# Performance work log

Measured on AMD Instinct MI355X. Metric: run time of the kernel, lower is better.

Reference implementation:

```python
import jax, jax.numpy as jnp
import numpy as np


def _ap_class_loss(s_plus, s_minus):
    """AP rank loss for one class.

    s_plus:  [P] positive scores sorted DESCENDING (grads flow through sort gather)
    s_minus: [N] negative scores sorted ASCENDING  (grads flow through sort gather)

    The original torch code computes the optimal interleaving rank of each
    negative with a recursive quickselect divide-and-conquer. Because the
    optimal rank is monotone in the negative's score (the property the
    divide-and-conquer exploits), each negative's rank can equivalently be
    computed independently: for the negative of ascending rank j (1-indexed),
    delta_k = 1/(P*(j+k)) - 2*(s_plus[k-1] - s_minus[j-1])/(P*N),  k=1..P,
    opt_j = argmax over r in [1, P+1] of sum_{k>=r} delta_k (first max on ties),
    which is exactly opt_j() evaluated on the full range.
    """
    P = s_plus.shape[0]
    N = s_minus.shape[0]
    Pf, Nf = float(P), float(N)
    j = jnp.arange(1, N + 1, dtype=jnp.float32)[:, None]   # [N,1] ascending rank
    k = jnp.arange(1, P + 1, dtype=jnp.float32)[None, :]   # [1,P]
    # delta[m, k-1] for negative m (ascending) vs positive k (descending)
    delta = (1.0 / (j + k)) / Pf - 2.0 * (s_plus[None, :] - s_minus[:, None]) / (Pf * Nf)
    dz = jnp.concatenate([delta, jnp.zeros((N, 1), delta.dtype)], axis=1)  # [N,P+1]
    # suffix[m, u] = sum_{i>=u} dz[m, i]  (matches flip-cumsum-flip in torch)
    suffix = jnp.cumsum(dz[:, ::-1], axis=1)[:, ::-1]
    opt = 1 + jnp.argmax(suffix, axis=1)                    # [N] int in [1, P+1]
    opt_f = jax.lax.stop_gradient(opt.astype(jnp.float32))
    # r_plus[i] = 1 + |{m : opt_m <= i+1}| via cumulative histogram of opt values
    hist = jnp.zeros(P + 2, jnp.float32).at[opt].add(1.0)
    cum = jnp.cumsum(hist)
    r_plus = 1.0 + cum[1:P + 1]                             # [P], thresholds 1..P
    i_arr = jnp.arange(P, dtype=jnp.float32)
    Delta_R_R_star = 1.0 - jnp.sum((i_arr + 1.0) / (i_arr + r_plus)) / Pf
    c_plus = Nf + 2.0 - 2.0 * r_plus                        # detached in torch
    c_minus = Pf + 2.0 - 2.0 * opt_f
    F_R = jnp.dot(s_plus, c_plus) + jnp.dot(s_minus, c_minus)
    # c_plus_star = N*ones, c_minus_star = -P*ones
    F_R_star = Nf * jnp.sum(s_plus) - Pf * jnp.sum(s_minus)
    return jax.lax.stop_gradient(Delta_R_R_star) + (F_R - F_R_star) / (Pf * Nf)


def _ap_loss(scores, pos_neg):
    total = jnp.zeros((), scores.dtype)
    for c, (pos, neg) in enumerate(pos_neg):
        if pos.size == 0 or neg.size == 0:
            continue  # torch returns 0 * s_plus.sum()
        col = scores[:, c]
        sp = col[pos]
        sm = col[neg]
        sp = sp[jnp.argsort(-sp)]   # descending; detached sort idx, grad via gather
        sm = sm[jnp.argsort(sm)]    # ascending (quickselect partial sort, same pairing)
        total = total + _ap_class_loss(sp, sm)
    return total / len(pos_neg)


def setup_inputs() -> dict:
    key = jax.random.key(0)
    k1, k2 = jax.random.split(key)
    C, n_classes = 16384, 16
    scores = jax.random.normal(k1, (C, n_classes), dtype=jnp.float32)
    class_labels = jax.random.randint(k2, (C,), 0, n_classes, dtype=jnp.int32)
    return {"scores": scores, "class_labels": class_labels}


def reference(scores, class_labels):
    labels = np.asarray(class_labels)
    n_classes = scores.shape[1]
    pos_neg = [(np.nonzero(labels == c)[0], np.nonzero(labels != c)[0])
               for c in range(n_classes)]
    return _ap_loss(scores, pos_neg)
```

## Files before the change

### kernel.cpp

```cpp
#include <hip/hip_runtime.h>
#include <stdint.h>

#define C_ITEMS 16384
#define NCLS 16
#define HSTRIDE 16386
#define NB 65536
#define BSH 16

static const size_t OFF_COL  = 0;
static const size_t OFF_SPOS = 1u << 20;
static const size_t OFF_SNEG = 2u << 20;
static const size_t OFF_PACK = 3u << 20;
static const size_t OFF_HIST = 4u << 20;
static const size_t OFF_CNT  = OFF_HIST + (size_t)NCLS * HSTRIDE * 4;
static const size_t OFF_ACCS = OFF_CNT + 64;
static const size_t OFF_ACCV = OFF_ACCS + 128;
static const size_t OFF_TOT  = OFF_ACCV + 128;
static const size_t OFF_PC   = OFF_TOT + 8;
static const size_t OFF_H1   = (OFF_PC + 64 + 255) & ~(size_t)255;
static const size_t ZERO_END = OFF_H1 + ((size_t)NCLS * NB * 4);
static const size_t ZERO_BYTES = ZERO_END - OFF_HIST;
static const size_t OFF_PPK  = 10u << 20;

__device__ __forceinline__ unsigned ordkey(float f) {
  unsigned b = __float_as_uint(f);
  return (b & 0x80000000u) ? ~b : (b | 0x80000000u);
}

__global__ void k_zero(unsigned* __restrict__ p, int n) {
  int stride = gridDim.x * blockDim.x;
  for (int t = blockIdx.x * blockDim.x + threadIdx.x; t < n; t += stride) p[t] = 0u;
}

__global__ void k_prep2(const float* __restrict__ scores, const int* __restrict__ labels,
                        float* __restrict__ col, unsigned* __restrict__ h1,
                        unsigned* __restrict__ pcnt, unsigned long long* __restrict__ ppk) {
  int t = blockIdx.x * 256 + threadIdx.x;
  float v = scores[t];
  int i = t >> 4, c = t & 15;
  col[(c << 14) | i] = v;
  if (labels[i] != c)
    atomicAdd(&h1[(c << 16) + (ordkey(v) >> BSH)], 1u);
  if (blockIdx.x < 64) {
    __shared__ unsigned lc[NCLS];
    __shared__ unsigned base[NCLS];
    int tid = threadIdx.x;
    if (tid < NCLS) lc[tid] = 0;
    __syncthreads();
    int ii = blockIdx.x * 256 + tid;
    int cc = labels[ii] & 15;
    float vv = scores[ii * NCLS + cc];
    unsigned loc = atomicAdd(&lc[cc], 1u);
    __syncthreads();
    if (tid < NCLS) base[tid] = lc[tid] ? atomicAdd(&pcnt[tid], lc[tid]) : 0u;
    __syncthreads();
    ppk[(cc << 14) + base[cc] + loc] = ((unsigned long long)(~ordkey(vv)) << 32) | (unsigned)ii;
  }
}

#define PCAP 2048
__global__ __launch_bounds__(1024) void k_mid(
    unsigned* __restrict__ h1, const float* __restrict__ col,
    const unsigned* __restrict__ pcnt, const unsigned long long* __restrict__ ppk,
    float* __restrict__ spos) {
  int b = blockIdx.x;
  int tid = threadIdx.x;
  __shared__ unsigned part[1024];
  __shared__ unsigned long long pk[PCAP];
  if (b < NCLS) {
    unsigned* h = h1 + ((size_t)b << 16);
    unsigned base = (unsigned)tid << 6;
    unsigned s = 0;
    for (int q = 0; q < 64; ++q) s += h[base + q];
    part[tid] = s;
    __syncthreads();
    for (int off = 1; off < 1024; off <<= 1) {
      unsigned v = (tid >= off) ? part[tid - off] : 0u;
      __syncthreads();
      part[tid] += v;
      __syncthreads();
    }
    unsigned running = part[tid] - s;
    for (int q = 0; q < 64; ++q) {
      unsigned tmp = h[base + q];
      h[base + q] = running;
      running += tmp;
    }
  } else {
    int c = b - NCLS;
    unsigned P = pcnt[c];
    const unsigned long long* src = ppk + ((size_t)c << 14);
    if (P <= PCAP) {
      for (unsigned t = tid; t < P; t += 1024) pk[t] = src[t];
      __syncthreads();
      for (unsigned q = tid; q < P; q += 1024) {
        unsigned long long k64 = pk[q];
        unsigned cq = 0;
        for (unsigned t = 0; t < P; ++t) cq += (pk[t] < k64) ? 1u : 0u;
        unsigned i = (unsigned)(k64 & 0xFFFFFFFFu);
        spos[(c << 14) + cq] = col[(c << 14) + (int)i];
      }
    } else {
      for (unsigned q = tid; q < P; q += 1024) {
        unsigned long long k64 = src[q];
        unsigned cq = 0;
        for (unsigned t = 0; t < P; ++t) cq += (src[t] < k64) ? 1u : 0u;
        unsigned i = (unsigned)(k64 & 0xFFFFFFFFu);
        spos[(c << 14) + cq] = col[(c << 14) + (int)i];
      }
    }
  }
}

__global__ void k_scatter(const float* __restrict__ col, const int* __restrict__ labels,
                          unsigned* __restrict__ h1, unsigned* __restrict__ pack) {
  int t = blockIdx.x * 256 + threadIdx.x;
  int c = t >> 14, i = t & 16383;
  if (labels[i] != c) {
    unsigned k = ordkey(col[t]);
    unsigned p = atomicAdd(&h1[(c << 16) + (k >> BSH)], 1u);
    pack[(c << 14) + p] = (k << 16) | (unsigned)i;
  }
}

__global__ void k_rankfine(const float* __restrict__ col, const int* __restrict__ labels,
                           const unsigned* __restrict__ h1, const unsigned* __restrict__ pack,
                           float* __restrict__ sneg) {
  int t = blockIdx.x * 256 + threadIdx.x;
  int c = t >> 14, i = t & 16383;
  if (labels[i] != c) {
    float v = col[t];
    unsigned k = ordkey(v);
    unsigned b = k >> BSH;
    const unsigned* hb = h1 + ((size_t)c << 16);
    unsigned start = b ? hb[b - 1] : 0u;
    unsigned end = hb[b];
    unsigned mine = (k << 16) | (unsigned)i;
    const unsigned* pk = pack + (c << 14);
    unsigned cnt = start;
    for (unsigned q = start; q < end; ++q) cnt += (pk[q] < mine) ? 1u : 0u;
    sneg[(c << 14) + (int)cnt] = v;
  }
}

#define SCAP 2048
#define HCAP 2048
#define ASTEP 64
#define ABITS 6

__global__ void k_anchor(const unsigned* __restrict__ counts, const float* __restrict__ spos,
                         const float* __restrict__ sneg, unsigned* __restrict__ aopt) {
  int c = blockIdx.y;
  int P = (int)counts[c];
  int N = C_ITEMS - P;
  if (P == 0 || N == 0) return;
  int tid = threadIdx.x;
  __shared__ float sp[SCAP];
  int stageN = (P <= SCAP) ? P : 0;
  for (int t = tid; t < stageN; t += 64) sp[t] = spos[(c << 14) + t];
  __syncthreads();
  int ta = blockIdx.x * 64 + tid;
  int T = (N + ASTEP - 1) / ASTEP + 1;
  if (ta >= T) return;
  float invP = 1.0f / (float)P;
  float coef = 2.0f / ((float)P * (float)N);
  int j0 = min(ta * ASTEP, N - 1);
  float v = sneg[(c << 14) + j0];
  float a = coef * v;
  float fcnt = (float)(j0 + P + 1);
  float s = 0.0f, best = 0.0f;
  int besti = P;
  if (P <= SCAP) {
    for (int q = P - 1; q >= 0; --q) {
      float spv = sp[q];
      float r = __builtin_amdgcn_rcpf(fcnt);
      float delta = fmaf(invP, r, fmaf(-coef, spv, a));
      s += delta;
      if (s >= best) { best = s; besti = q; }
      fcnt -= 1.0f;
    }
  } else {
    const float* spg = spos + ((size_t)c << 14);
    for (int q = P - 1; q >= 0; --q) {
      float spv = spg[q];
      float r = __builtin_amdgcn_rcpf(fcnt);
      float delta = fmaf(invP, r, fmaf(-coef, spv, a));
      s += delta;
      if (s >= best) { best = s; besti = q; }
      fcnt -= 1.0f;
    }
  }
  aopt[(c << 9) + ta] = (unsigned)(besti + 1);
}

__global__ void k_optB(const unsigned* __restrict__ counts, const float* __restrict__ spos,
                       const float* __restrict__ sneg, const unsigned* __restrict__ aopt,
                       unsigned* __restrict__ hist, double* __restrict__ accS,
                       double* __restrict__ accV) {
  int c = blockIdx.y;
  int P = (int)counts[c];
  int N = C_ITEMS - P;
  if (P == 0 || N == 0) return;
  int tid = threadIdx.x;
  int j0 = blockIdx.x * 256 + tid;
  bool active = (j0 < N);
  __shared__ float sp[SCAP];
  __shared__ unsigned lh[HCAP];
  __shared__ double red[256];
  int stageN = (P <= SCAP) ? P : 0;
  int zn = (P + 2 <= HCAP) ? (P + 2) : 0;
  for (int t = tid; t < stageN; t += 256) sp[t] = spos[(c << 14) + t];
  for (int t = tid; t < zn; t += 256) lh[t] = 0u;
  __syncthreads();
  int opt = P + 1;
  float v = 0.0f;
  if (active) {
    v = sneg[(c << 14) + j0];
    int g = j0 >> ABITS;
    int hiA = (int)aopt[(c << 9) + g];
    if ((j0 & (ASTEP - 1)) == 0) {
      opt = hiA;
    } else {
      int loA = (int)aopt[(c << 9) + g + 1];
      int hi = min(hiA + 2, P + 1);
      int lo = max(loA - 2, 1);
      float invP = 1.0f / (float)P;
      float coef = 2.0f / ((float)P * (float)N);
      float a = coef * v;
      float s = 0.0f, best = 0.0f;
      int bestr = hi;
      float fcnt = (float)(j0 + hi);
      if (P <= SCAP) {
        for (int k = hi - 1; k >= lo; --k) {
          float spv = sp[k - 1];
          float r = __builtin_amdgcn_rcpf(fcnt);
          float delta = fmaf(invP, r, fmaf(-coef, spv, a));
          s += delta;
          if (s >= best) { best = s; bestr = k; }
          fcnt -= 1.0f;
        }
      } else {
        const float* spg = spos + ((size_t)c << 14);
        for (int k = hi - 1; k >= lo; --k) {
          float spv = spg[k - 1];
          float r = __builtin_amdgcn_rcpf(fcnt);
          float delta = fmaf(invP, r, fmaf(-coef, spv, a));
          s += delta;
          if (s >= best) { best = s; bestr = k; }
          fcnt -= 1.0f;
        }
      }
      opt = bestr;
    }
  }
  if (P + 2 <= HCAP) {
    if (active) atomicAdd(&lh[opt], 1u);
    __syncthreads();
    for (int t = tid; t < P + 2; t += 256)
      if (lh[t]) atomicAdd(&hist[c * HSTRIDE + t], lh[t]);
  } else {
    if (active) atomicAdd(&hist[c * HSTRIDE + opt], 1u);
  }
  double cm = active ? (double)(P + 2 - 2 * opt) * (double)v : 0.0;
  double sv = active ? (double)v : 0.0;
  red[tid] = cm; __syncthreads();
  for (int sh = 128; sh > 0; sh >>= 1) { if (tid < sh) red[tid] += red[tid + sh]; __syncthreads(); }
  if (tid == 0) atomicAdd(&accS[c], red[0]);
  __syncthreads();
  red[tid] = sv; __syncthreads();
  for (int sh = 128; sh > 0; sh >>= 1) { if (tid < sh) red[tid] += red[tid + sh]; __syncthreads(); }
  if (tid == 0) atomicAdd(&accV[c], red[0]);
}

__global__ void k_fin(const unsigned* __restrict__ counts, const unsigned* __restrict__ hist,
                      const float* __restrict__ spos, const double* __restrict__ accS,
                      const double* __restrict__ accV, double* __restrict__ total,
                      unsigned* __restrict__ done, float* __restrict__ out) {
  int c = blockIdx.x;
  int tid = threadIdx.x;
  int P = (int)counts[c];
  int N = C_ITEMS - P;
  __shared__ unsigned sc[256];
  __shared__ double red[256];
  double lc = 0.0;
  if (P > 0 && N > 0) {
    const unsigned* h = hist + c * HSTRIDE;
    int M = P + 1;
    int L = (M + 255) / 256;
    int o0 = 1 + tid * L;
    int o1 = min(o0 + L, P + 2);
    unsigned part = 0;
    for (int o = o0; o < o1; ++o) part += h[o];
    sc[tid] = part;
    __syncthreads();
    if (tid == 0) {
      unsigned runp = 0;
      for (int t = 0; t < 256; ++t) { unsigned tmp = sc[t]; sc[t] = runp; runp += tmp; }
    }
    __syncthreads();
    unsigned run = sc[tid];
    double a1 = 0.0, a2 = 0.0, a3 = 0.0;
    for (int o = o0; o < o1; ++o) {
      run += h[o];
      if (o <= P) {
        int k0 = o - 1;
        double rp = 1.0 + (double)run;
        double spv = (double)spos[(c << 14) + k0];
        a1 += (double)(k0 + 1) / ((double)k0 + rp);
        a2 += spv * ((double)N + 2.0 - 2.0 * rp);
        a3 += spv;
      }
    }
    red[tid] = a1; __syncthreads();
    for (int s = 128; s > 0; s >>= 1) { if (tid < s) red[tid] += red[tid + s]; __syncthreads(); }
    double r1 = red[0]; __syncthreads();
    red[tid] = a2; __syncthreads();
    for (int s = 128; s > 0; s >>= 1) { if (tid < s) red[tid] += red[tid + s]; __syncthreads(); }
    double r2 = red[0]; __syncthreads();
    red[tid] = a3; __syncthreads();
    for (int s = 128; s > 0; s >>= 1) { if (tid < s) red[tid] += red[tid + s]; __syncthreads(); }
    double r3 = red[0];
    if (tid == 0) {
      double Pd = (double)P, Nd = (double)N;
      double FR  = r2 + accS[c];
      double FRs = Nd * r3 - Pd * accV[c];
      lc = (1.0 - r1 / Pd) + (FR - FRs) / (Pd * Nd);
    }
  }
  if (tid == 0) {
    if (P > 0 && N > 0) atomicAdd(total, lc);
    __threadfence();
    unsigned d = atomicAdd(done, 1u);
    if (d == NCLS - 1) {
      double t = atomicAdd(total, 0.0);
      out[0] = (float)(t / (double)NCLS);
    }
  }
}

extern "C" void kernel_launch(void* const* d_in, const int* in_sizes, int n_in,
                              void* d_out, int out_size, void* d_ws, size_t ws_size,
                              hipStream_t stream) {
  (void)in_sizes; (void)n_in; (void)out_size; (void)ws_size;
  const float* scores = (const float*)d_in[0];
  const int* labels = (const int*)d_in[1];
  float* out = (float*)d_out;
  char* ws = (char*)d_ws;
  float* col      = (float*)(ws + OFF_COL);
  float* spos     = (float*)(ws + OFF_SPOS);
  float* sneg     = (float*)(ws + OFF_SNEG);
  unsigned* pack  = (unsigned*)(ws + OFF_PACK);
  unsigned* hist  = (unsigned*)(ws + OFF_HIST);
  unsigned* done  = (unsigned*)(ws + OFF_CNT);
  double* accS    = (double*)(ws + OFF_ACCS);
  double* accV    = (double*)(ws + OFF_ACCV);
  double* total   = (double*)(ws + OFF_TOT);
  unsigned* pcnt  = (unsigned*)(ws + OFF_PC);
  unsigned* h1    = (unsigned*)(ws + OFF_H1);
  unsigned long long* ppk = (unsigned long long*)(ws + OFF_PPK);
  unsigned* aopt  = (unsigned*)(ws + OFF_PPK);

  int zn = (int)(ZERO_BYTES / 4);
  k_zero<<<1024, 256, 0, stream>>>(hist, zn);
  k_prep2<<<1024, 256, 0, stream>>>(scores, labels, col, h1, pcnt, ppk);
  k_mid<<<32, 1024, 0, stream>>>(h1, col, pcnt, ppk, spos);
  k_scatter<<<1024, 256, 0, stream>>>(col, labels, h1, pack);
  k_rankfine<<<1024, 256, 0, stream>>>(col, labels, h1, pack, sneg);
  k_anchor<<<dim3(5, NCLS), 64, 0, stream>>>(pcnt, spos, sneg, aopt);
  k_optB<<<dim3(64, NCLS), 256, 0, stream>>>(pcnt, spos, sneg, aopt, hist, accS, accV);
  k_fin<<<NCLS, 256, 0, stream>>>(pcnt, hist, spos, accS, accV, total, done, out);
}
```

Baseline: 196.6 us.

## Fuse final per-class reduction into optB via last-block-done counter

The separate k_fin launch is removed. The last block of each class in the opt kernel, found with a per-class atomic counter and a threadfence, now does the histogram prefix scan and computes the class loss. A second counter picks the last class to write the output. This saves one kernel launch and its dependency gap, at the cost of atomic reads of the histogram and serial finalisation work in one block per class.

```diff
diff --git a/kernel.cpp b/kernel.cpp
--- a/kernel.cpp
+++ b/kernel.cpp
@@ -13,7 +13,8 @@
 static const size_t OFF_PACK = 3u << 20;
 static const size_t OFF_HIST = 4u << 20;
 static const size_t OFF_CNT  = OFF_HIST + (size_t)NCLS * HSTRIDE * 4;
-static const size_t OFF_ACCS = OFF_CNT + 64;
+static const size_t OFF_DC   = OFF_CNT + 64;
+static const size_t OFF_ACCS = OFF_CNT + 128;
 static const size_t OFF_ACCV = OFF_ACCS + 128;
 static const size_t OFF_TOT  = OFF_ACCV + 128;
 static const size_t OFF_PC   = OFF_TOT + 8;
@@ -193,21 +194,24 @@
   aopt[(c << 9) + ta] = (unsigned)(besti + 1);
 }
 
-__global__ void k_optB(const unsigned* __restrict__ counts, const float* __restrict__ spos,
-                       const float* __restrict__ sneg, const unsigned* __restrict__ aopt,
-                       unsigned* __restrict__ hist, double* __restrict__ accS,
-                       double* __restrict__ accV) {
+__global__ void k_optB3(const unsigned* __restrict__ counts, const float* __restrict__ spos,
+                        const float* __restrict__ sneg, const unsigned* __restrict__ aopt,
+                        unsigned* __restrict__ hist, double* __restrict__ accS,
+                        double* __restrict__ accV, double* __restrict__ total,
+                        unsigned* __restrict__ cnt, unsigned* __restrict__ dcls,
+                        float* __restrict__ out) {
   int c = blockIdx.y;
   int P = (int)counts[c];
   int N = C_ITEMS - P;
-  if (P == 0 || N == 0) return;
+  bool valid = (P > 0 && N > 0);
   int tid = threadIdx.x;
   int j0 = blockIdx.x * 256 + tid;
-  bool active = (j0 < N);
+  bool active = valid && (j0 < N);
   __shared__ float sp[SCAP];
   __shared__ unsigned lh[HCAP];
   __shared__ double red[256];
-  int stageN = (P <= SCAP) ? P : 0;
+  __shared__ int lastFlag;
+  int stageN = (valid && P <= SCAP) ? P : 0;
   int zn = (P + 2 <= HCAP) ? (P + 2) : 0;
   for (int t = tid; t < stageN; t += 256) sp[t] = spos[(c << 14) + t];
   for (int t = tid; t < zn; t += 256) lh[t] = 0u;
@@ -265,75 +269,73 @@
   double sv = active ? (double)v : 0.0;
   red[tid] = cm; __syncthreads();
   for (int sh = 128; sh > 0; sh >>= 1) { if (tid < sh) red[tid] += red[tid + sh]; __syncthreads(); }
-  if (tid == 0) atomicAdd(&accS[c], red[0]);
+  if (tid == 0 && valid) atomicAdd(&accS[c], red[0]);
   __syncthreads();
   red[tid] = sv; __syncthreads();
   for (int sh = 128; sh > 0; sh >>= 1) { if (tid < sh) red[tid] += red[tid + sh]; __syncthreads(); }
-  if (tid == 0) atomicAdd(&accV[c], red[0]);
-}
-
-__global__ void k_fin(const unsigned* __restrict__ counts, const unsigned* __restrict__ hist,
-                      const float* __restrict__ spos, const double* __restrict__ accS,
-                      const double* __restrict__ accV, double* __restrict__ total,
-                      unsigned* __restrict__ done, float* __restrict__ out) {
-  int c = blockIdx.x;
-  int tid = threadIdx.x;
-  int P = (int)counts[c];
-  int N = C_ITEMS - P;
-  __shared__ unsigned sc[256];
-  __shared__ double red[256];
-  double lc = 0.0;
-  if (P > 0 && N > 0) {
-    const unsigned* h = hist + c * HSTRIDE;
-    int M = P + 1;
-    int L = (M + 255) / 256;
-    int o0 = 1 + tid * L;
-    int o1 = min(o0 + L, P + 2);
-    unsigned part = 0;
-    for (int o = o0; o < o1; ++o) part += h[o];
-    sc[tid] = part;
-    __syncthreads();
+  if (tid == 0 && valid) atomicAdd(&accV[c], red[0]);
+
+  if (tid == 0) {
+    __threadfence();
+    unsigned d = atomicAdd(&cnt[c], 1u);
+    lastFlag = (d == (unsigned)(gridDim.x - 1)) ? 1 : 0;
+  }
+  __syncthreads();
+  if (lastFlag) {
+    double lc = 0.0;
+    unsigned* hC = hist + c * HSTRIDE;
+    if (valid) {
+      __shared__ unsigned sc[256];
+      int M = P + 1;
+      int L = (M + 255) / 256;
+      int o0 = 1 + tid * L;
+      int o1 = min(o0 + L, P + 2);
+      unsigned part = 0;
+      for (int o = o0; o < o1; ++o) part += atomicAdd(&hC[o], 0u);
+      sc[tid] = part;
+      __syncthreads();
+      if (tid == 0) {
+        unsigned runp = 0;
+        for (int t = 0; t < 256; ++t) { unsigned tmp = sc[t]; sc[t] = runp; runp += tmp; }
+      }
+      __syncthreads();
+      unsigned run = sc[tid];
+      double a1 = 0.0, a2 = 0.0, a3 = 0.0;
+      for (int o = o0; o < o1; ++o) {
+        run += atomicAdd(&hC[o], 0u);
+        if (o <= P) {
+          int k0 = o - 1;
+          double rp = 1.0 + (double)run;
+          double spv = (double)spos[(c << 14) + k0];
+          a1 += (double)(k0 + 1) / ((double)k0 + rp);
+          a2 += spv * ((double)N + 2.0 - 2.0 * rp);
+          a3 += spv;
+        }
+      }
+      red[tid] = a1; __syncthreads();
+      for (int s = 128; s > 0; s >>= 1) { if (tid < s) red[tid] += red[tid + s]; __syncthreads(); }
+      double r1 = red[0]; __syncthreads();
+      red[tid] = a2; __syncthreads();
+      for (int s = 128; s > 0; s >>= 1) { if (tid < s) red[tid] += red[tid + s]; __syncthreads(); }
+      double r2 = red[0]; __syncthreads();
+      red[tid] = a3; __syncthreads();
+      for (int s = 128; s > 0; s >>= 1) { if (tid < s) red[tid] += red[tid + s]; __syncthreads(); }
+      double r3 = red[0];
+      if (tid == 0) {
+        double Pd = (double)P, Nd = (double)N;
+        double FR  = r2 + atomicAdd(&accS[c], 0.0);
+        double FRs = Nd * r3 - Pd * atomicAdd(&accV[c], 0.0);
+        lc = (1.0 - r1 / Pd) + (FR - FRs) / (Pd * Nd);
+      }
+    }
     if (tid == 0) {
-      unsigned runp = 0;
-      for (int t = 0; t < 256; ++t) { unsigned tmp = sc[t]; sc[t] = runp; runp += tmp; }
-    }
-    __syncthreads();
-    unsigned run = sc[tid];
-    double a1 = 0.0, a2 = 0.0, a3 = 0.0;
-    for (int o = o0; o < o1; ++o) {
-      run += h[o];
-      if (o <= P) {
-        int k0 = o - 1;
-        double rp = 1.0 + (double)run;
-        double spv = (double)spos[(c << 14) + k0];
-        a1 += (double)(k0 + 1) / ((double)k0 + rp);
-        a2 += spv * ((double)N + 2.0 - 2.0 * rp);
-        a3 += spv;
-      }
-    }
-    red[tid] = a1; __syncthreads();
-    for (int s = 128; s > 0; s >>= 1) { if (tid < s) red[tid] += red[tid + s]; __syncthreads(); }
-    double r1 = red[0]; __syncthreads();
-    red[tid] = a2; __syncthreads();
-    for (int s = 128; s > 0; s >>= 1) { if (tid < s) red[tid] += red[tid + s]; __syncthreads(); }
-    double r2 = red[0]; __syncthreads();
-    red[tid] = a3; __syncthreads();
-    for (int s = 128; s > 0; s >>= 1) { if (tid < s) red[tid] += red[tid + s]; __syncthreads(); }
-    double r3 = red[0];
-    if (tid == 0) {
-      double Pd = (double)P, Nd = (double)N;
-      double FR  = r2 + accS[c];
-      double FRs = Nd * r3 - Pd * accV[c];
-      lc = (1.0 - r1 / Pd) + (FR - FRs) / (Pd * Nd);
-    }
-  }
-  if (tid == 0) {
-    if (P > 0 && N > 0) atomicAdd(total, lc);
-    __threadfence();
-    unsigned d = atomicAdd(done, 1u);
-    if (d == NCLS - 1) {
-      double t = atomicAdd(total, 0.0);
-      out[0] = (float)(t / (double)NCLS);
+      if (valid) atomicAdd(total, lc);
+      __threadfence();
+      unsigned dd = atomicAdd(dcls, 1u);
+      if (dd == NCLS - 1) {
+        double t = atomicAdd(total, 0.0);
+        out[0] = (float)(t / (double)NCLS);
+      }
     }
   }
 }
@@ -351,7 +353,8 @@
   float* sneg     = (float*)(ws + OFF_SNEG);
   unsigned* pack  = (unsigned*)(ws + OFF_PACK);
   unsigned* hist  = (unsigned*)(ws + OFF_HIST);
-  unsigned* done  = (unsigned*)(ws + OFF_CNT);
+  unsigned* cnt   = (unsigned*)(ws + OFF_CNT);
+  unsigned* dcls  = (unsigned*)(ws + OFF_DC);
   double* accS    = (double*)(ws + OFF_ACCS);
   double* accV    = (double*)(ws + OFF_ACCV);
   double* total   = (double*)(ws + OFF_TOT);
@@ -367,6 +370,6 @@
   k_scatter<<<1024, 256, 0, stream>>>(col, labels, h1, pack);
   k_rankfine<<<1024, 256, 0, stream>>>(col, labels, h1, pack, sneg);
   k_anchor<<<dim3(5, NCLS), 64, 0, stream>>>(pcnt, spos, sneg, aopt);
-  k_optB<<<dim3(64, NCLS), 256, 0, stream>>>(pcnt, spos, sneg, aopt, hist, accS, accV);
-  k_fin<<<NCLS, 256, 0, stream>>>(pcnt, hist, spos, accS, accV, total, done, out);
-}
+  k_optB3<<<dim3(64, NCLS), 256, 0, stream>>>(pcnt, spos, sneg, aopt, hist, accS, accV,
+                                              total, cnt, dcls, out);
+}
```

Measured after the change: 209.4 us. 1.07x slower.
